# Performance work log

Hardware: AMD Instinct MI355X
Metric: run time of the kernel (lower is better)

The kernel has to match this reference:

```python
import jax, jax.numpy as jnp
import numpy as np

B, S, I, H = 128, 512, 256, 512


def _lstm_last_hidden(x, W_ih, W_hh, b_ih, b_hh):
    """Single-layer unidirectional LSTM (PyTorch gate order i,f,g,o).
    x: [B,S,I]; returns final hidden state h_n [B,H]."""
    Hd = W_hh.shape[1]
    # Precompute input-side gate activations for all timesteps: [S,B,4H]
    xg = jnp.einsum('bsi,gi->sbg', x, W_ih) + b_ih + b_hh

    def step(carry, gx):
        h, c = carry
        g = gx + h @ W_hh.T  # [B,4H]
        i, f, gg, o = jnp.split(g, 4, axis=-1)
        i = jax.nn.sigmoid(i)
        f = jax.nn.sigmoid(f)
        gg = jnp.tanh(gg)
        o = jax.nn.sigmoid(o)
        c = f * c + i * gg
        h = o * jnp.tanh(c)
        return (h, c), None

    h0 = jnp.zeros((x.shape[0], Hd), x.dtype)
    (h_n, _), _ = jax.lax.scan(step, (h0, h0), xg)
    return h_n


def setup_inputs() -> dict:
    key = jax.random.key(0)
    k1, k2, k3, k4, k5, k6 = jax.random.split(key, 6)
    s = 1.0 / np.sqrt(H)  # PyTorch LSTM init scale
    return {
        'text_one': jax.random.normal(k1, (B, S, I), jnp.float32),
        'text_two': jax.random.normal(k2, (B, S, I), jnp.float32),
        'W_ih': jax.random.normal(k3, (4 * H, I), jnp.float32) * s,
        'W_hh': jax.random.normal(k4, (4 * H, H), jnp.float32) * s,
        'b_ih': jax.random.normal(k5, (4 * H,), jnp.float32) * s,
        'b_hh': jax.random.normal(k6, (4 * H,), jnp.float32) * s,
    }


def reference(text_one, text_two, W_ih, W_hh, b_ih, b_hh):
    out1 = _lstm_last_hidden(text_one, W_ih, W_hh, b_ih, b_hh)
    out2 = _lstm_last_hidden(text_two, W_ih, W_hh, b_ih, b_hh)
    return (out1, out2)
```

## Files before the change

kernel.cpp:

```cpp
#include <hip/hip_runtime.h>
#include <stdint.h>

#define SLEN    512
#define IDIM    256
#define HDIM    512
#define NROW    256
#define KP      776
#define NSTEP   512
#define NGRP    16
#define GWG     16

typedef __attribute__((ext_vector_type(8))) _Float16 half8;
typedef __attribute__((ext_vector_type(4))) float   f32x4;
typedef __attribute__((ext_vector_type(4))) int     i32x4;

__device__ __forceinline__ float sigm(float x)   { return 1.0f / (1.0f + __expf(-x)); }
__device__ __forceinline__ float tanh_f(float x) { return 2.0f / (1.0f + __expf(-2.0f * x)) - 1.0f; }

__device__ __forceinline__ half8 cvt8(float4 a, float4 b) {
    half8 v;
    v[0] = (_Float16)a.x; v[1] = (_Float16)a.y; v[2] = (_Float16)a.z; v[3] = (_Float16)a.w;
    v[4] = (_Float16)b.x; v[5] = (_Float16)b.y; v[6] = (_Float16)b.z; v[7] = (_Float16)b.w;
    return v;
}

union hu { _Float16 h; unsigned short u; };

__global__ __launch_bounds__(256, 1)
void lstm_persistent(const float* __restrict__ x0, const float* __restrict__ x1,
                     const float* __restrict__ wih, const float* __restrict__ whh,
                     const float* __restrict__ bih, const float* __restrict__ bhh,
                     _Float16* __restrict__ hb, int* __restrict__ flg,
                     float* __restrict__ out) {
    __shared__ __align__(16) _Float16 Ab[16 * KP];

    const int tid  = threadIdx.x;
    const int lane = tid & 63;
    const int w    = tid >> 6;
    const int quad = lane >> 4;
    const int l16  = lane & 15;
    const int igrp = blockIdx.x & 15;
    const int jcg  = blockIdx.x >> 4;

    const int q0  = l16 & 3, ccl = l16 >> 2;
    const int colb = jcg * 32 + w * 8 + ccl * 2;
    const int gc0 = q0 * HDIM + colb;
    const int gc1 = gc0 + 1;
    half8 wf0[24], wf1[24];
#pragma unroll
    for (int kk = 0; kk < 24; ++kk) {
        int k0 = kk * 32 + quad * 8;
        const float* sA = (k0 < IDIM) ? wih + (size_t)gc0 * IDIM + k0
                                      : whh + (size_t)gc0 * HDIM + (k0 - IDIM);
        const float* sB = (k0 < IDIM) ? wih + (size_t)gc1 * IDIM + k0
                                      : whh + (size_t)gc1 * HDIM + (k0 - IDIM);
        wf0[kk] = cvt8(*(const float4*)sA, *(const float4*)(sA + 4));
        wf1[kk] = cvt8(*(const float4*)sB, *(const float4*)(sB + 4));
    }

    float bias0[4], bias1[4];
#pragma unroll
    for (int q = 0; q < 4; ++q) {
        int g0 = q * HDIM + jcg * 32 + w * 8 + quad * 2;
        bias0[q] = bih[g0] + bhh[g0];
        bias1[q] = bih[g0 + 1] + bhh[g0 + 1];
    }

    const float* xp  = (igrp < 8) ? x0 : x1;
    const int   brow = (igrp & 7) * 16;
    const int   r0   = tid >> 5;
    const int   o0   = (tid & 31) * 8;
    const int   grow = igrp * 16 + l16;
    const int   cc0  = jcg * 32 + w * 8 + quad * 2;

    const int* fpoll = flg + igrp * 64 + lane;
    int*       fmine = flg + igrp * 64 + jcg * 4 + w;

    float c0 = 0.f, c1 = 0.f;
    int gaveup = 0;

    {
        const float* xr0 = xp + ((size_t)(brow + r0) * SLEN + 0) * IDIM + o0;
        const float* xr1 = xr0 + (size_t)8 * SLEN * IDIM;
        float4 pa = *(const float4*)xr0, pb = *(const float4*)(xr0 + 4);
        float4 pc = *(const float4*)xr1, pd = *(const float4*)(xr1 + 4);
        *(half8*)&Ab[r0 * KP + o0]       = cvt8(pa, pb);
        *(half8*)&Ab[(r0 + 8) * KP + o0] = cvt8(pc, pd);
    }

#pragma unroll 1
    for (int t = 0; t < NSTEP; ++t) {
        __syncthreads();

        f32x4 acc0 = {bias0[0], bias0[1], bias0[2], bias0[3]};
        f32x4 acc1 = {bias1[0], bias1[1], bias1[2], bias1[3]};

        float4 pa, pb, pc, pd;
        if (t < NSTEP - 1) {
            const float* xr0 = xp + ((size_t)(brow + r0) * SLEN + (t + 1)) * IDIM + o0;
            const float* xr1 = xr0 + (size_t)8 * SLEN * IDIM;
            pa = *(const float4*)xr0; pb = *(const float4*)(xr0 + 4);
            pc = *(const float4*)xr1; pd = *(const float4*)(xr1 + 4);
        }

        const _Float16* ab = &Ab[l16 * KP + quad * 8];
#pragma unroll
        for (int kk = 0; kk < 8; ++kk) {
            half8 bf = *(const half8*)(ab + kk * 32);
            acc0 = __builtin_amdgcn_mfma_f32_16x16x32_f16(wf0[kk], bf, acc0, 0, 0, 0);
            acc1 = __builtin_amdgcn_mfma_f32_16x16x32_f16(wf1[kk], bf, acc1, 0, 0, 0);
        }

        if (t > 0 && !gaveup) {
            int it = 0;
            while (true) {
                int f;
                asm volatile("global_load_dword %0, %1, off sc0 sc1\n\t"
                             "s_waitcnt vmcnt(0)"
                             : "=v"(f) : "v"(fpoll) : "memory");
                if (__all(f >= t)) break;
                __builtin_amdgcn_s_sleep(1);
                if (++it > (1 << 20)) { gaveup = 1; break; }
            }
            __builtin_amdgcn_fence(__ATOMIC_ACQUIRE, "workgroup");
        }

        {
            const char* hs = (const char*)
                (hb + (size_t)((t + 1) & 1) * (NROW * HDIM) + (size_t)(igrp * 16) * HDIM);
            i32x4 v0_, v1_, v2_, v3_;
            asm volatile(
                "global_load_dwordx4 %0, %4, off sc0 sc1\n\t"
                "global_load_dwordx4 %1, %5, off sc0 sc1\n\t"
                "global_load_dwordx4 %2, %6, off sc0 sc1\n\t"
                "global_load_dwordx4 %3, %7, off sc0 sc1\n\t"
                "s_waitcnt vmcnt(0)"
                : "=&v"(v0_), "=&v"(v1_), "=&v"(v2_), "=&v"(v3_)
                : "v"(hs + (size_t)(tid      ) * 16), "v"(hs + (size_t)(tid + 256) * 16),
                  "v"(hs + (size_t)(tid + 512) * 16), "v"(hs + (size_t)(tid + 768) * 16)
                : "memory");
            *(i32x4*)&Ab[((tid      ) >> 6) * KP + IDIM + ((tid      ) & 63) * 8] = v0_;
            *(i32x4*)&Ab[((tid + 256) >> 6) * KP + IDIM + ((tid + 256) & 63) * 8] = v1_;
            *(i32x4*)&Ab[((tid + 512) >> 6) * KP + IDIM + ((tid + 512) & 63) * 8] = v2_;
            *(i32x4*)&Ab[((tid + 768) >> 6) * KP + IDIM + ((tid + 768) & 63) * 8] = v3_;
        }
        __syncthreads();

#pragma unroll
        for (int kk = 8; kk < 24; ++kk) {
            half8 bf = *(const half8*)(ab + kk * 32);
            acc0 = __builtin_amdgcn_mfma_f32_16x16x32_f16(wf0[kk], bf, acc0, 0, 0, 0);
            acc1 = __builtin_amdgcn_mfma_f32_16x16x32_f16(wf1[kk], bf, acc1, 0, 0, 0);
        }

        float i0 = sigm(acc0[0]), f0 = sigm(acc0[1]), g0 = tanh_f(acc0[2]), o0g = sigm(acc0[3]);
        c0 = f0 * c0 + i0 * g0;
        float h0 = o0g * tanh_f(c0);
        float i1 = sigm(acc1[0]), f1 = sigm(acc1[1]), g1 = tanh_f(acc1[2]), o1g = sigm(acc1[3]);
        c1 = f1 * c1 + i1 * g1;
        float h1 = o1g * tanh_f(c1);

        if (t < NSTEP - 1) {
            *(half8*)&Ab[r0 * KP + o0]       = cvt8(pa, pb);
            *(half8*)&Ab[(r0 + 8) * KP + o0] = cvt8(pc, pd);

            _Float16* hd = hb + (size_t)(t & 1) * (NROW * HDIM) + (size_t)grow * HDIM;
            hu u0; u0.h = (_Float16)h0;
            hu u1; u1.h = (_Float16)h1;
            unsigned int hp = (unsigned int)u0.u | ((unsigned int)u1.u << 16);
            asm volatile(
                "global_store_dword %0, %1, off sc0 sc1\n\t"
                "s_waitcnt vmcnt(0)"
                :: "v"((int*)(hd + cc0)), "v"(hp)
                : "memory");
            if (lane == 0) {
                int fv = t + 1;
                asm volatile("global_store_dword %0, %1, off sc0 sc1"
                             :: "v"(fmine), "v"(fv) : "memory");
            }
        } else {
            float2 ov; ov.x = h0; ov.y = h1;
            *(float2*)(out + (size_t)grow * HDIM + cc0) = ov;
        }
    }
}

extern "C" void kernel_launch(void* const* d_in, const int* in_sizes, int n_in,
                              void* d_out, int out_size, void* d_ws, size_t ws_size,
                              hipStream_t stream) {
    const float* x0  = (const float*)d_in[0];
    const float* x1  = (const float*)d_in[1];
    const float* wih = (const float*)d_in[2];
    const float* whh = (const float*)d_in[3];
    const float* bih = (const float*)d_in[4];
    const float* bhh = (const float*)d_in[5];

    _Float16* hb = (_Float16*)d_ws;
    int* flg = (int*)((char*)d_ws + (size_t)2 * NROW * HDIM * sizeof(_Float16));
    size_t zbytes = (size_t)2 * NROW * HDIM * sizeof(_Float16)
                  + (size_t)NGRP * 64 * sizeof(int);
    hipMemsetAsync(d_ws, 0, zbytes, stream);

    lstm_persistent<<<dim3(256), dim3(256), 0, stream>>>(
        x0, x1, wih, whh, bih, bhh, hb, flg, (float*)d_out);
}
```

Before: 1.743 ms.

## Interleave two batch groups per workgroup to hide cross-block sync latency

Each persistent workgroup now handles two 16-row batch groups, alternating between them, with the grid halved to 128 blocks and LDS doubled. While one group waits on its flag, the other group's compute proceeds. The flag for the next group is prefetched asynchronously, and flag stores are deferred. The h-state copy now uses global_load_lds directly into shared memory instead of register staging. This hides the inter-block polling and global-memory latency of the recurrent dependency, at the cost of serializing twice the MFMA work per block and adding more complex synchronization ordering.

```diff
diff --git a/kernel.cpp b/kernel.cpp
--- a/kernel.cpp
+++ b/kernel.cpp
@@ -12,7 +12,6 @@
 
 typedef __attribute__((ext_vector_type(8))) _Float16 half8;
 typedef __attribute__((ext_vector_type(4))) float   f32x4;
-typedef __attribute__((ext_vector_type(4))) int     i32x4;
 
 __device__ __forceinline__ float sigm(float x)   { return 1.0f / (1.0f + __expf(-x)); }
 __device__ __forceinline__ float tanh_f(float x) { return 2.0f / (1.0f + __expf(-2.0f * x)) - 1.0f; }
@@ -32,15 +31,15 @@
                      const float* __restrict__ bih, const float* __restrict__ bhh,
                      _Float16* __restrict__ hb, int* __restrict__ flg,
                      float* __restrict__ out) {
-    __shared__ __align__(16) _Float16 Ab[16 * KP];
+    __shared__ __align__(16) _Float16 Ab[2][16 * KP];
 
     const int tid  = threadIdx.x;
     const int lane = tid & 63;
     const int w    = tid >> 6;
     const int quad = lane >> 4;
     const int l16  = lane & 15;
-    const int igrp = blockIdx.x & 15;
-    const int jcg  = blockIdx.x >> 4;
+    const int pair = blockIdx.x & 7;
+    const int jcg  = blockIdx.x >> 3;
 
     const int q0  = l16 & 3, ccl = l16 >> 2;
     const int colb = jcg * 32 + w * 8 + ccl * 2;
@@ -66,121 +65,126 @@
         bias1[q] = bih[g0 + 1] + bhh[g0 + 1];
     }
 
-    const float* xp  = (igrp < 8) ? x0 : x1;
-    const int   brow = (igrp & 7) * 16;
-    const int   r0   = tid >> 5;
-    const int   o0   = (tid & 31) * 8;
-    const int   grow = igrp * 16 + l16;
-    const int   cc0  = jcg * 32 + w * 8 + quad * 2;
-
-    const int* fpoll = flg + igrp * 64 + lane;
-    int*       fmine = flg + igrp * 64 + jcg * 4 + w;
-
-    float c0 = 0.f, c1 = 0.f;
+    const int r0  = tid >> 5;
+    const int o0  = (tid & 31) * 8;
+    const int cc0 = jcg * 32 + w * 8 + quad * 2;
+
+    const int igrps[2] = { pair * 2, pair * 2 + 1 };
+    const float* xps[2];
+    xps[0] = (igrps[0] < 8) ? x0 : x1;
+    xps[1] = (igrps[1] < 8) ? x0 : x1;
+    const int brows[2] = { (igrps[0] & 7) * 16, (igrps[1] & 7) * 16 };
+    const int grows[2] = { igrps[0] * 16 + l16, igrps[1] * 16 + l16 };
+    const int* fpolls[2] = { flg + igrps[0] * 64 + lane, flg + igrps[1] * 64 + lane };
+    int* fmines[2] = { flg + igrps[0] * 64 + jcg * 4 + w,
+                       flg + igrps[1] * 64 + jcg * 4 + w };
+
+    float cr0[2] = {0.f, 0.f}, cr1[2] = {0.f, 0.f};
+    int pf = 0;
     int gaveup = 0;
 
-    {
-        const float* xr0 = xp + ((size_t)(brow + r0) * SLEN + 0) * IDIM + o0;
+#pragma unroll
+    for (int s = 0; s < 2; ++s) {
+        const float* xr0 = xps[s] + ((size_t)(brows[s] + r0) * SLEN + 0) * IDIM + o0;
         const float* xr1 = xr0 + (size_t)8 * SLEN * IDIM;
         float4 pa = *(const float4*)xr0, pb = *(const float4*)(xr0 + 4);
         float4 pc = *(const float4*)xr1, pd = *(const float4*)(xr1 + 4);
-        *(half8*)&Ab[r0 * KP + o0]       = cvt8(pa, pb);
-        *(half8*)&Ab[(r0 + 8) * KP + o0] = cvt8(pc, pd);
-    }
+        *(half8*)&Ab[s][r0 * KP + o0]       = cvt8(pa, pb);
+        *(half8*)&Ab[s][(r0 + 8) * KP + o0] = cvt8(pc, pd);
+    }
+    __syncthreads();
 
 #pragma unroll 1
     for (int t = 0; t < NSTEP; ++t) {
-        __syncthreads();
-
-        f32x4 acc0 = {bias0[0], bias0[1], bias0[2], bias0[3]};
-        f32x4 acc1 = {bias1[0], bias1[1], bias1[2], bias1[3]};
-
-        float4 pa, pb, pc, pd;
-        if (t < NSTEP - 1) {
-            const float* xr0 = xp + ((size_t)(brow + r0) * SLEN + (t + 1)) * IDIM + o0;
-            const float* xr1 = xr0 + (size_t)8 * SLEN * IDIM;
-            pa = *(const float4*)xr0; pb = *(const float4*)(xr0 + 4);
-            pc = *(const float4*)xr1; pd = *(const float4*)(xr1 + 4);
-        }
-
-        const _Float16* ab = &Ab[l16 * KP + quad * 8];
-#pragma unroll
-        for (int kk = 0; kk < 8; ++kk) {
-            half8 bf = *(const half8*)(ab + kk * 32);
-            acc0 = __builtin_amdgcn_mfma_f32_16x16x32_f16(wf0[kk], bf, acc0, 0, 0, 0);
-            acc1 = __builtin_amdgcn_mfma_f32_16x16x32_f16(wf1[kk], bf, acc1, 0, 0, 0);
-        }
-
-        if (t > 0 && !gaveup) {
-            int it = 0;
-            while (true) {
-                int f;
-                asm volatile("global_load_dword %0, %1, off sc0 sc1\n\t"
-                             "s_waitcnt vmcnt(0)"
-                             : "=v"(f) : "v"(fpoll) : "memory");
-                if (__all(f >= t)) break;
-                __builtin_amdgcn_s_sleep(1);
-                if (++it > (1 << 20)) { gaveup = 1; break; }
-            }
-            __builtin_amdgcn_fence(__ATOMIC_ACQUIRE, "workgroup");
-        }
-
-        {
-            const char* hs = (const char*)
-                (hb + (size_t)((t + 1) & 1) * (NROW * HDIM) + (size_t)(igrp * 16) * HDIM);
-            i32x4 v0_, v1_, v2_, v3_;
-            asm volatile(
-                "global_load_dwordx4 %0, %4, off sc0 sc1\n\t"
-                "global_load_dwordx4 %1, %5, off sc0 sc1\n\t"
-                "global_load_dwordx4 %2, %6, off sc0 sc1\n\t"
-                "global_load_dwordx4 %3, %7, off sc0 sc1\n\t"
-                "s_waitcnt vmcnt(0)"
-                : "=&v"(v0_), "=&v"(v1_), "=&v"(v2_), "=&v"(v3_)
-                : "v"(hs + (size_t)(tid      ) * 16), "v"(hs + (size_t)(tid + 256) * 16),
-                  "v"(hs + (size_t)(tid + 512) * 16), "v"(hs + (size_t)(tid + 768) * 16)
-                : "memory");
-            *(i32x4*)&Ab[((tid      ) >> 6) * KP + IDIM + ((tid      ) & 63) * 8] = v0_;
-            *(i32x4*)&Ab[((tid + 256) >> 6) * KP + IDIM + ((tid + 256) & 63) * 8] = v1_;
-            *(i32x4*)&Ab[((tid + 512) >> 6) * KP + IDIM + ((tid + 512) & 63) * 8] = v2_;
-            *(i32x4*)&Ab[((tid + 768) >> 6) * KP + IDIM + ((tid + 768) & 63) * 8] = v3_;
-        }
-        __syncthreads();
-
-#pragma unroll
-        for (int kk = 8; kk < 24; ++kk) {
-            half8 bf = *(const half8*)(ab + kk * 32);
-            acc0 = __builtin_amdgcn_mfma_f32_16x16x32_f16(wf0[kk], bf, acc0, 0, 0, 0);
-            acc1 = __builtin_amdgcn_mfma_f32_16x16x32_f16(wf1[kk], bf, acc1, 0, 0, 0);
-        }
-
-        float i0 = sigm(acc0[0]), f0 = sigm(acc0[1]), g0 = tanh_f(acc0[2]), o0g = sigm(acc0[3]);
-        c0 = f0 * c0 + i0 * g0;
-        float h0 = o0g * tanh_f(c0);
-        float i1 = sigm(acc1[0]), f1 = sigm(acc1[1]), g1 = tanh_f(acc1[2]), o1g = sigm(acc1[3]);
-        c1 = f1 * c1 + i1 * g1;
-        float h1 = o1g * tanh_f(c1);
-
-        if (t < NSTEP - 1) {
-            *(half8*)&Ab[r0 * KP + o0]       = cvt8(pa, pb);
-            *(half8*)&Ab[(r0 + 8) * KP + o0] = cvt8(pc, pd);
-
-            _Float16* hd = hb + (size_t)(t & 1) * (NROW * HDIM) + (size_t)grow * HDIM;
-            hu u0; u0.h = (_Float16)h0;
-            hu u1; u1.h = (_Float16)h1;
-            unsigned int hp = (unsigned int)u0.u | ((unsigned int)u1.u << 16);
-            asm volatile(
-                "global_store_dword %0, %1, off sc0 sc1\n\t"
-                "s_waitcnt vmcnt(0)"
-                :: "v"((int*)(hd + cc0)), "v"(hp)
-                : "memory");
-            if (lane == 0) {
-                int fv = t + 1;
+#pragma unroll
+        for (int s = 0; s < 2; ++s) {
+            if (!(t == 0 && s == 0)) {
+                asm volatile("s_waitcnt vmcnt(0)" ::: "memory");
+                __builtin_amdgcn_sched_barrier(0);
+                if (lane == 0) {
+                    int fv = s ? (t + 1) : t;
+                    asm volatile("global_store_dword %0, %1, off sc0 sc1"
+                                 :: "v"(fmines[1 - s]), "v"(fv) : "memory");
+                }
+            }
+            if (t > 0 && !gaveup) {
+                if (!__all(pf >= t)) {
+                    int it = 0;
+                    while (true) {
+                        int f;
+                        asm volatile("global_load_dword %0, %1, off sc0 sc1\n\t"
+                                     "s_waitcnt vmcnt(0)"
+                                     : "=v"(f) : "v"(fpolls[s]) : "memory");
+                        if (__all(f >= t)) break;
+                        __builtin_amdgcn_s_sleep(1);
+                        if (++it > (1 << 20)) { gaveup = 1; break; }
+                    }
+                }
+                __builtin_amdgcn_fence(__ATOMIC_ACQUIRE, "workgroup");
+            }
+            {
+                const _Float16* hsrc = hb + (size_t)((t + 1) & 1) * (NROW * HDIM)
+                                          + (size_t)(igrps[s] * 16) * HDIM;
+#pragma unroll
+                for (int p = 0; p < 4; ++p) {
+                    const int r = p * 4 + w;
+                    const _Float16* g = hsrc + (size_t)r * HDIM + lane * 8;
+                    __builtin_amdgcn_global_load_lds(
+                        (const __attribute__((address_space(1))) void*)g,
+                        (__attribute__((address_space(3))) void*)&Ab[s][r * KP + IDIM],
+                        16, 0, 17 );
+                }
+            }
+            float4 pa, pb, pc, pd;
+            if (t < NSTEP - 1) {
+                const float* xr0 = xps[s] + ((size_t)(brows[s] + r0) * SLEN + (t + 1)) * IDIM + o0;
+                const float* xr1 = xr0 + (size_t)8 * SLEN * IDIM;
+                pa = *(const float4*)xr0; pb = *(const float4*)(xr0 + 4);
+                pc = *(const float4*)xr1; pd = *(const float4*)(xr1 + 4);
+            }
+            f32x4 acc0 = {bias0[0], bias0[1], bias0[2], bias0[3]};
+            f32x4 acc1 = {bias1[0], bias1[1], bias1[2], bias1[3]};
+            const _Float16* ab = &Ab[s][l16 * KP + quad * 8];
+#pragma unroll
+            for (int kk = 0; kk < 8; ++kk) {
+                half8 bf = *(const half8*)(ab + kk * 32);
+                acc0 = __builtin_amdgcn_mfma_f32_16x16x32_f16(wf0[kk], bf, acc0, 0, 0, 0);
+                acc1 = __builtin_amdgcn_mfma_f32_16x16x32_f16(wf1[kk], bf, acc1, 0, 0, 0);
+            }
+            asm volatile("s_waitcnt vmcnt(0)" ::: "memory");
+            __builtin_amdgcn_sched_barrier(0);
+            __syncthreads();
+#pragma unroll
+            for (int kk = 8; kk < 24; ++kk) {
+                half8 bf = *(const half8*)(ab + kk * 32);
+                acc0 = __builtin_amdgcn_mfma_f32_16x16x32_f16(wf0[kk], bf, acc0, 0, 0, 0);
+                acc1 = __builtin_amdgcn_mfma_f32_16x16x32_f16(wf1[kk], bf, acc1, 0, 0, 0);
+            }
+            float i0 = sigm(acc0[0]), f0 = sigm(acc0[1]), g0 = tanh_f(acc0[2]), o0g = sigm(acc0[3]);
+            cr0[s] = f0 * cr0[s] + i0 * g0;
+            float h0 = o0g * tanh_f(cr0[s]);
+            float i1 = sigm(acc1[0]), f1 = sigm(acc1[1]), g1 = tanh_f(acc1[2]), o1g = sigm(acc1[3]);
+            cr1[s] = f1 * cr1[s] + i1 * g1;
+            float h1 = o1g * tanh_f(cr1[s]);
+
+            if (t < NSTEP - 1) {
+                _Float16* hd = hb + (size_t)(t & 1) * (NROW * HDIM) + (size_t)grows[s] * HDIM;
+                hu u0; u0.h = (_Float16)h0;
+                hu u1; u1.h = (_Float16)h1;
+                unsigned int hp = (unsigned int)u0.u | ((unsigned int)u1.u << 16);
                 asm volatile("global_store_dword %0, %1, off sc0 sc1"
-                             :: "v"(fmine), "v"(fv) : "memory");
-            }
-        } else {
-            float2 ov; ov.x = h0; ov.y = h1;
-            *(float2*)(out + (size_t)grow * HDIM + cc0) = ov;
+                             :: "v"((int*)(hd + cc0)), "v"(hp) : "memory");
+                *(half8*)&Ab[s][r0 * KP + o0]       = cvt8(pa, pb);
+                *(half8*)&Ab[s][(r0 + 8) * KP + o0] = cvt8(pc, pd);
+            } else {
+                float2 ov; ov.x = h0; ov.y = h1;
+                *(float2*)(out + (size_t)grows[s] * HDIM + cc0) = ov;
+            }
+            if (!(t == NSTEP - 1 && s == 1)) {
+                asm volatile("v_mov_b32 %0, 0\n\t"
+                             "global_load_dword %0, %1, off sc0 sc1"
+                             : "=&v"(pf) : "v"(fpolls[1 - s]) : "memory");
+            }
         }
     }
 }
@@ -201,6 +205,6 @@
                   + (size_t)NGRP * 64 * sizeof(int);
     hipMemsetAsync(d_ws, 0, zbytes, stream);
 
-    lstm_persistent<<<dim3(256), dim3(256), 0, stream>>>(
+    lstm_persistent<<<dim3(128), dim3(256), 0, stream>>>(
         x0, x1, wih, whh, bih, bhh, hb, flg, (float*)d_out);
 }
```

Result: slower. 2.475 ms (+42.0%).

## Embed step tags with hidden-state values to replace separate flag polling

Applied to the files above, without the earlier changes.

Each exchanged hidden-state pair is now stored together with its timestep tag in one 8-byte store. Consumers poll the data itself until every tag matches, so the separate flag store/poll round trip and the store-side wait are gone. The next x-slice prefetch is moved after the first MFMA block and issued via inline asm, and __syncthreads is replaced by explicit lgkmcnt waits plus s_barrier. The cost is twice the exchange traffic per step, since each 2-byte-pair payload now carries 4 bytes of tag. The give-up threshold is also lowered.

```diff
diff --git a/kernel.cpp b/kernel.cpp
--- a/kernel.cpp
+++ b/kernel.cpp
@@ -9,10 +9,12 @@
 #define NSTEP   512
 #define NGRP    16
 #define GWG     16
+#define EXCH    256
 
 typedef __attribute__((ext_vector_type(8))) _Float16 half8;
 typedef __attribute__((ext_vector_type(4))) float   f32x4;
 typedef __attribute__((ext_vector_type(4))) int     i32x4;
+typedef __attribute__((ext_vector_type(2))) int     i32x2;
 
 __device__ __forceinline__ float sigm(float x)   { return 1.0f / (1.0f + __expf(-x)); }
 __device__ __forceinline__ float tanh_f(float x) { return 2.0f / (1.0f + __expf(-2.0f * x)) - 1.0f; }
@@ -23,6 +25,10 @@
     v[4] = (_Float16)b.x; v[5] = (_Float16)b.y; v[6] = (_Float16)b.z; v[7] = (_Float16)b.w;
     return v;
 }
+__device__ __forceinline__ half8 cvt8i(i32x4 a, i32x4 b) {
+    float4 fa = *(float4*)&a, fb = *(float4*)&b;
+    return cvt8(fa, fb);
+}
 
 union hu { _Float16 h; unsigned short u; };
 
@@ -30,8 +36,7 @@
 void lstm_persistent(const float* __restrict__ x0, const float* __restrict__ x1,
                      const float* __restrict__ wih, const float* __restrict__ whh,
                      const float* __restrict__ bih, const float* __restrict__ bhh,
-                     _Float16* __restrict__ hb, int* __restrict__ flg,
-                     float* __restrict__ out) {
+                     char* __restrict__ exb, float* __restrict__ out) {
     __shared__ __align__(16) _Float16 Ab[16 * KP];
 
     const int tid  = threadIdx.x;
@@ -73,8 +78,8 @@
     const int   grow = igrp * 16 + l16;
     const int   cc0  = jcg * 32 + w * 8 + quad * 2;
 
-    const int* fpoll = flg + igrp * 64 + lane;
-    int*       fmine = flg + igrp * 64 + jcg * 4 + w;
+    const int rr = tid >> 4;
+    const int cb = (tid & 15) * 16;
 
     float c0 = 0.f, c1 = 0.f;
     int gaveup = 0;
@@ -87,22 +92,16 @@
         *(half8*)&Ab[r0 * KP + o0]       = cvt8(pa, pb);
         *(half8*)&Ab[(r0 + 8) * KP + o0] = cvt8(pc, pd);
     }
+    __syncthreads();
 
 #pragma unroll 1
     for (int t = 0; t < NSTEP; ++t) {
-        __syncthreads();
+        asm volatile("s_waitcnt lgkmcnt(0)" ::: "memory");
+        __builtin_amdgcn_sched_barrier(0);
+        __builtin_amdgcn_s_barrier();
 
         f32x4 acc0 = {bias0[0], bias0[1], bias0[2], bias0[3]};
         f32x4 acc1 = {bias1[0], bias1[1], bias1[2], bias1[3]};
-
-        float4 pa, pb, pc, pd;
-        if (t < NSTEP - 1) {
-            const float* xr0 = xp + ((size_t)(brow + r0) * SLEN + (t + 1)) * IDIM + o0;
-            const float* xr1 = xr0 + (size_t)8 * SLEN * IDIM;
-            pa = *(const float4*)xr0; pb = *(const float4*)(xr0 + 4);
-            pc = *(const float4*)xr1; pd = *(const float4*)(xr1 + 4);
-        }
-
         const _Float16* ab = &Ab[l16 * KP + quad * 8];
 #pragma unroll
         for (int kk = 0; kk < 8; ++kk) {
@@ -111,40 +110,70 @@
             acc1 = __builtin_amdgcn_mfma_f32_16x16x32_f16(wf1[kk], bf, acc1, 0, 0, 0);
         }
 
-        if (t > 0 && !gaveup) {
+        i32x4 xv0, xv1, xv2, xv3;
+        if (t < NSTEP - 1) {
+            const float* xr0 = xp + ((size_t)(brow + r0) * SLEN + (t + 1)) * IDIM + o0;
+            const float* xr1 = xr0 + (size_t)8 * SLEN * IDIM;
+            asm volatile(
+                "global_load_dwordx4 %0, %4, off\n\t"
+                "global_load_dwordx4 %1, %4, off offset:16\n\t"
+                "global_load_dwordx4 %2, %5, off\n\t"
+                "global_load_dwordx4 %3, %5, off offset:16"
+                : "=&v"(xv0), "=&v"(xv1), "=&v"(xv2), "=&v"(xv3)
+                : "v"(xr0), "v"(xr1)
+                : "memory");
+        }
+
+        i32x4 L0, L1, L2, L3, L4, L5, L6, L7;
+        {
+            const char* base = exb
+                + ((size_t)(((t + 1) & 1) * NROW + igrp * 16 + rr) * EXCH + cb) * 8;
             int it = 0;
             while (true) {
-                int f;
-                asm volatile("global_load_dword %0, %1, off sc0 sc1\n\t"
-                             "s_waitcnt vmcnt(0)"
-                             : "=v"(f) : "v"(fpoll) : "memory");
-                if (__all(f >= t)) break;
+                asm volatile(
+                    "global_load_dwordx4 %0, %8, off sc0 sc1\n\t"
+                    "global_load_dwordx4 %1, %8, off offset:16 sc0 sc1\n\t"
+                    "global_load_dwordx4 %2, %8, off offset:32 sc0 sc1\n\t"
+                    "global_load_dwordx4 %3, %8, off offset:48 sc0 sc1\n\t"
+                    "global_load_dwordx4 %4, %8, off offset:64 sc0 sc1\n\t"
+                    "global_load_dwordx4 %5, %8, off offset:80 sc0 sc1\n\t"
+                    "global_load_dwordx4 %6, %8, off offset:96 sc0 sc1\n\t"
+                    "global_load_dwordx4 %7, %8, off offset:112 sc0 sc1\n\t"
+                    "s_waitcnt vmcnt(0)"
+                    : "=&v"(L0), "=&v"(L1), "=&v"(L2), "=&v"(L3),
+                      "=&v"(L4), "=&v"(L5), "=&v"(L6), "=&v"(L7)
+                    : "v"(base)
+                    : "memory");
+                int ok = (L0[1] == t) & (L0[3] == t) & (L1[1] == t) & (L1[3] == t)
+                       & (L2[1] == t) & (L2[3] == t) & (L3[1] == t) & (L3[3] == t)
+                       & (L4[1] == t) & (L4[3] == t) & (L5[1] == t) & (L5[3] == t)
+                       & (L6[1] == t) & (L6[3] == t) & (L7[1] == t) & (L7[3] == t);
+                if (__all(ok)) break;
                 __builtin_amdgcn_s_sleep(1);
-                if (++it > (1 << 20)) { gaveup = 1; break; }
+                if (++it > (1 << 16)) { gaveup = 1; break; }
             }
             __builtin_amdgcn_fence(__ATOMIC_ACQUIRE, "workgroup");
-        }
-
-        {
-            const char* hs = (const char*)
-                (hb + (size_t)((t + 1) & 1) * (NROW * HDIM) + (size_t)(igrp * 16) * HDIM);
-            i32x4 v0_, v1_, v2_, v3_;
-            asm volatile(
-                "global_load_dwordx4 %0, %4, off sc0 sc1\n\t"
-                "global_load_dwordx4 %1, %5, off sc0 sc1\n\t"
-                "global_load_dwordx4 %2, %6, off sc0 sc1\n\t"
-                "global_load_dwordx4 %3, %7, off sc0 sc1\n\t"
-                "s_waitcnt vmcnt(0)"
-                : "=&v"(v0_), "=&v"(v1_), "=&v"(v2_), "=&v"(v3_)
-                : "v"(hs + (size_t)(tid      ) * 16), "v"(hs + (size_t)(tid + 256) * 16),
-                  "v"(hs + (size_t)(tid + 512) * 16), "v"(hs + (size_t)(tid + 768) * 16)
-                : "memory");
-            *(i32x4*)&Ab[((tid      ) >> 6) * KP + IDIM + ((tid      ) & 63) * 8] = v0_;
-            *(i32x4*)&Ab[((tid + 256) >> 6) * KP + IDIM + ((tid + 256) & 63) * 8] = v1_;
-            *(i32x4*)&Ab[((tid + 512) >> 6) * KP + IDIM + ((tid + 512) & 63) * 8] = v2_;
-            *(i32x4*)&Ab[((tid + 768) >> 6) * KP + IDIM + ((tid + 768) & 63) * 8] = v3_;
-        }
-        __syncthreads();
+            i32x2 s0; s0[0] = L0[0]; s0[1] = L0[2];
+            i32x2 s1; s1[0] = L1[0]; s1[1] = L1[2];
+            i32x2 s2; s2[0] = L2[0]; s2[1] = L2[2];
+            i32x2 s3; s3[0] = L3[0]; s3[1] = L3[2];
+            i32x2 s4; s4[0] = L4[0]; s4[1] = L4[2];
+            i32x2 s5; s5[0] = L5[0]; s5[1] = L5[2];
+            i32x2 s6; s6[0] = L6[0]; s6[1] = L6[2];
+            i32x2 s7; s7[0] = L7[0]; s7[1] = L7[2];
+            _Float16* hrow = &Ab[rr * KP + IDIM + 2 * cb];
+            *(i32x2*)(hrow +  0) = s0;
+            *(i32x2*)(hrow +  4) = s1;
+            *(i32x2*)(hrow +  8) = s2;
+            *(i32x2*)(hrow + 12) = s3;
+            *(i32x2*)(hrow + 16) = s4;
+            *(i32x2*)(hrow + 20) = s5;
+            *(i32x2*)(hrow + 24) = s6;
+            *(i32x2*)(hrow + 28) = s7;
+        }
+        asm volatile("s_waitcnt lgkmcnt(0)" ::: "memory");
+        __builtin_amdgcn_sched_barrier(0);
+        __builtin_amdgcn_s_barrier();
 
 #pragma unroll
         for (int kk = 8; kk < 24; ++kk) {
@@ -161,27 +190,21 @@
         float h1 = o1g * tanh_f(c1);
 
         if (t < NSTEP - 1) {
-            *(half8*)&Ab[r0 * KP + o0]       = cvt8(pa, pb);
-            *(half8*)&Ab[(r0 + 8) * KP + o0] = cvt8(pc, pd);
-
-            _Float16* hd = hb + (size_t)(t & 1) * (NROW * HDIM) + (size_t)grow * HDIM;
             hu u0; u0.h = (_Float16)h0;
             hu u1; u1.h = (_Float16)h1;
-            unsigned int hp = (unsigned int)u0.u | ((unsigned int)u1.u << 16);
-            asm volatile(
-                "global_store_dword %0, %1, off sc0 sc1\n\t"
-                "s_waitcnt vmcnt(0)"
-                :: "v"((int*)(hd + cc0)), "v"(hp)
-                : "memory");
-            if (lane == 0) {
-                int fv = t + 1;
-                asm volatile("global_store_dword %0, %1, off sc0 sc1"
-                             :: "v"(fmine), "v"(fv) : "memory");
-            }
+            i32x2 sv;
+            sv[0] = (int)((unsigned int)u0.u | ((unsigned int)u1.u << 16));
+            sv[1] = t + 1;
+            char* dst = exb + ((size_t)((t & 1) * NROW + grow) * EXCH + (cc0 >> 1)) * 8;
+            asm volatile("global_store_dwordx2 %0, %1, off sc0 sc1"
+                         :: "v"(dst), "v"(sv) : "memory");
+            *(half8*)&Ab[r0 * KP + o0]       = cvt8i(xv0, xv1);
+            *(half8*)&Ab[(r0 + 8) * KP + o0] = cvt8i(xv2, xv3);
         } else {
             float2 ov; ov.x = h0; ov.y = h1;
             *(float2*)(out + (size_t)grow * HDIM + cc0) = ov;
         }
+        if (gaveup) break;
     }
 }
 
@@ -195,12 +218,10 @@
     const float* bih = (const float*)d_in[4];
     const float* bhh = (const float*)d_in[5];
 
-    _Float16* hb = (_Float16*)d_ws;
-    int* flg = (int*)((char*)d_ws + (size_t)2 * NROW * HDIM * sizeof(_Float16));
-    size_t zbytes = (size_t)2 * NROW * HDIM * sizeof(_Float16)
-                  + (size_t)NGRP * 64 * sizeof(int);
+    char* exb = (char*)d_ws;
+    size_t zbytes = (size_t)2 * NROW * EXCH * 8;
     hipMemsetAsync(d_ws, 0, zbytes, stream);
 
     lstm_persistent<<<dim3(256), dim3(256), 0, stream>>>(
-        x0, x1, wih, whh, bih, bhh, hb, flg, (float*)d_out);
-}
+        x0, x1, wih, whh, bih, bhh, exb, (float*)d_out);
+}
```

Measured after the change: 2.284 ms. 1.31x slower.

## Load recurrent h directly into LDS and defer next-step x prefetch

Applied to the files above, without the earlier changes.

Replaces the register-staged global loads of the shared hidden state with global_load_lds (direct-to-LDS) transfers. Moves the next-timestep x prefetch to after the h load, so its latency overlaps the second MFMA phase and the gate math. Also swaps __syncthreads for explicit waitcnt plus s_barrier with sched barriers, and publishes the flag before writing x into LDS. This shortens the per-step critical path of the cross-workgroup recurrence, but relies on hand-ordered waits and barriers, which makes correctness fragile.

```diff
diff --git a/kernel.cpp b/kernel.cpp
--- a/kernel.cpp
+++ b/kernel.cpp
@@ -14,6 +14,9 @@
 typedef __attribute__((ext_vector_type(4))) float   f32x4;
 typedef __attribute__((ext_vector_type(4))) int     i32x4;
 
+#define AS1 __attribute__((address_space(1)))
+#define AS3 __attribute__((address_space(3)))
+
 __device__ __forceinline__ float sigm(float x)   { return 1.0f / (1.0f + __expf(-x)); }
 __device__ __forceinline__ float tanh_f(float x) { return 2.0f / (1.0f + __expf(-2.0f * x)) - 1.0f; }
 
@@ -22,6 +25,10 @@
     v[0] = (_Float16)a.x; v[1] = (_Float16)a.y; v[2] = (_Float16)a.z; v[3] = (_Float16)a.w;
     v[4] = (_Float16)b.x; v[5] = (_Float16)b.y; v[6] = (_Float16)b.z; v[7] = (_Float16)b.w;
     return v;
+}
+__device__ __forceinline__ half8 cvt8i(i32x4 a, i32x4 b) {
+    float4 fa = *(float4*)&a, fb = *(float4*)&b;
+    return cvt8(fa, fb);
 }
 
 union hu { _Float16 h; unsigned short u; };
@@ -87,22 +94,18 @@
         *(half8*)&Ab[r0 * KP + o0]       = cvt8(pa, pb);
         *(half8*)&Ab[(r0 + 8) * KP + o0] = cvt8(pc, pd);
     }
+    __syncthreads();
 
 #pragma unroll 1
     for (int t = 0; t < NSTEP; ++t) {
-        __syncthreads();
+        if (t > 0) {
+            asm volatile("s_waitcnt lgkmcnt(0)" ::: "memory");
+            __builtin_amdgcn_sched_barrier(0);
+            __builtin_amdgcn_s_barrier();
+        }
 
         f32x4 acc0 = {bias0[0], bias0[1], bias0[2], bias0[3]};
         f32x4 acc1 = {bias1[0], bias1[1], bias1[2], bias1[3]};
-
-        float4 pa, pb, pc, pd;
-        if (t < NSTEP - 1) {
-            const float* xr0 = xp + ((size_t)(brow + r0) * SLEN + (t + 1)) * IDIM + o0;
-            const float* xr1 = xr0 + (size_t)8 * SLEN * IDIM;
-            pa = *(const float4*)xr0; pb = *(const float4*)(xr0 + 4);
-            pc = *(const float4*)xr1; pd = *(const float4*)(xr1 + 4);
-        }
-
         const _Float16* ab = &Ab[l16 * KP + quad * 8];
 #pragma unroll
         for (int kk = 0; kk < 8; ++kk) {
@@ -117,7 +120,7 @@
                 int f;
                 asm volatile("global_load_dword %0, %1, off sc0 sc1\n\t"
                              "s_waitcnt vmcnt(0)"
-                             : "=v"(f) : "v"(fpoll) : "memory");
+                             : "=&v"(f) : "v"(fpoll) : "memory");
                 if (__all(f >= t)) break;
                 __builtin_amdgcn_s_sleep(1);
                 if (++it > (1 << 20)) { gaveup = 1; break; }
@@ -126,25 +129,35 @@
         }
 
         {
-            const char* hs = (const char*)
-                (hb + (size_t)((t + 1) & 1) * (NROW * HDIM) + (size_t)(igrp * 16) * HDIM);
-            i32x4 v0_, v1_, v2_, v3_;
+            const _Float16* hsrc = hb + (size_t)((t + 1) & 1) * (NROW * HDIM)
+                                      + (size_t)(igrp * 16) * HDIM;
+#pragma unroll
+            for (int p = 0; p < 4; ++p) {
+                const int r = p * 4 + w;
+                const _Float16* g = hsrc + (size_t)r * HDIM + lane * 8;
+                __builtin_amdgcn_global_load_lds(
+                    (const AS1 void*)g, (AS3 void*)&Ab[r * KP + IDIM],
+                    16, 0, 17);
+            }
+            asm volatile("s_waitcnt vmcnt(0)" ::: "memory");
+            __builtin_amdgcn_sched_barrier(0);
+        }
+
+        i32x4 xv0, xv1, xv2, xv3;
+        if (t < NSTEP - 1) {
+            const float* xr0 = xp + ((size_t)(brow + r0) * SLEN + (t + 1)) * IDIM + o0;
+            const float* xr1 = xr0 + (size_t)8 * SLEN * IDIM;
             asm volatile(
-                "global_load_dwordx4 %0, %4, off sc0 sc1\n\t"
-                "global_load_dwordx4 %1, %5, off sc0 sc1\n\t"
-                "global_load_dwordx4 %2, %6, off sc0 sc1\n\t"
-                "global_load_dwordx4 %3, %7, off sc0 sc1\n\t"
-                "s_waitcnt vmcnt(0)"
-                : "=&v"(v0_), "=&v"(v1_), "=&v"(v2_), "=&v"(v3_)
-                : "v"(hs + (size_t)(tid      ) * 16), "v"(hs + (size_t)(tid + 256) * 16),
-                  "v"(hs + (size_t)(tid + 512) * 16), "v"(hs + (size_t)(tid + 768) * 16)
+                "global_load_dwordx4 %0, %4, off\n\t"
+                "global_load_dwordx4 %1, %4, off offset:16\n\t"
+                "global_load_dwordx4 %2, %5, off\n\t"
+                "global_load_dwordx4 %3, %5, off offset:16"
+                : "=&v"(xv0), "=&v"(xv1), "=&v"(xv2), "=&v"(xv3)
+                : "v"(xr0), "v"(xr1)
                 : "memory");
-            *(i32x4*)&Ab[((tid      ) >> 6) * KP + IDIM + ((tid      ) & 63) * 8] = v0_;
-            *(i32x4*)&Ab[((tid + 256) >> 6) * KP + IDIM + ((tid + 256) & 63) * 8] = v1_;
-            *(i32x4*)&Ab[((tid + 512) >> 6) * KP + IDIM + ((tid + 512) & 63) * 8] = v2_;
-            *(i32x4*)&Ab[((tid + 768) >> 6) * KP + IDIM + ((tid + 768) & 63) * 8] = v3_;
-        }
-        __syncthreads();
+        }
+        __builtin_amdgcn_sched_barrier(0);
+        __builtin_amdgcn_s_barrier();
 
 #pragma unroll
         for (int kk = 8; kk < 24; ++kk) {
@@ -161,23 +174,22 @@
         float h1 = o1g * tanh_f(c1);
 
         if (t < NSTEP - 1) {
-            *(half8*)&Ab[r0 * KP + o0]       = cvt8(pa, pb);
-            *(half8*)&Ab[(r0 + 8) * KP + o0] = cvt8(pc, pd);
-
             _Float16* hd = hb + (size_t)(t & 1) * (NROW * HDIM) + (size_t)grow * HDIM;
             hu u0; u0.h = (_Float16)h0;
             hu u1; u1.h = (_Float16)h1;
             unsigned int hp = (unsigned int)u0.u | ((unsigned int)u1.u << 16);
-            asm volatile(
-                "global_store_dword %0, %1, off sc0 sc1\n\t"
-                "s_waitcnt vmcnt(0)"
-                :: "v"((int*)(hd + cc0)), "v"(hp)
-                : "memory");
+            asm volatile("global_store_dword %0, %1, off sc0 sc1"
+                         :: "v"((int*)(hd + cc0)), "v"(hp) : "memory");
+            __builtin_amdgcn_sched_barrier(0);
+            asm volatile("s_waitcnt vmcnt(0)" ::: "memory");
+            __builtin_amdgcn_sched_barrier(0);
             if (lane == 0) {
                 int fv = t + 1;
                 asm volatile("global_store_dword %0, %1, off sc0 sc1"
                              :: "v"(fmine), "v"(fv) : "memory");
             }
+            *(half8*)&Ab[r0 * KP + o0]       = cvt8i(xv0, xv1);
+            *(half8*)&Ab[(r0 + 8) * KP + o0] = cvt8i(xv2, xv3);
         } else {
             float2 ov; ov.x = h0; ov.y = h1;
             *(float2*)(out + (size_t)grow * HDIM + cc0) = ov;
```

Result: faster. 1.563 ms (-10.3%).
